# Kernel optimization log

Hardware: AMD Instinct MI355X
Metric: run time of the kernel (lower is better)

## Reference

```python
import jax, jax.numpy as jnp
import numpy as np

NUM_LAYERS = 3
HIDDEN = 64
NUM_CLASSES = 4096
LN_EPS = 1e-5


def setup_inputs() -> dict:
    key = jax.random.key(0)
    ks = jax.random.split(key, 8)
    B, N, E, H = 8, NUM_CLASSES, 131072, HIDDEN
    node_features = jax.random.normal(ks[0], (B, N, H), dtype=jnp.float32)
    edge_indices = jax.random.randint(ks[1], (B, 2, E), 0, N, dtype=jnp.int64)
    edge_attrs = jax.random.normal(ks[2], (B, E, H), dtype=jnp.float32)
    # GraphConvolutionLayer params (xavier_uniform weight, zero bias) per layer
    limit = np.sqrt(6.0 / (H + H)).astype(np.float32)
    W = jax.random.uniform(ks[3], (NUM_LAYERS, H, H), minval=-limit, maxval=limit, dtype=jnp.float32)
    b = jnp.zeros((NUM_LAYERS, H), dtype=jnp.float32)
    gamma = jnp.ones((NUM_LAYERS, H), dtype=jnp.float32)
    beta = jnp.zeros((NUM_LAYERS, H), dtype=jnp.float32)
    global_emb = 0.02 * jax.random.normal(ks[4], (N, H), dtype=jnp.float32)
    return {
        "node_features": node_features,
        "edge_indices": edge_indices,
        "edge_attrs": edge_attrs,
        "W": W,
        "b": b,
        "gamma": gamma,
        "beta": beta,
        "global_emb": global_emb,
    }


def _layer_norm(x, g, bt):
    mu = jnp.mean(x, axis=-1, keepdims=True)
    var = jnp.mean((x - mu) ** 2, axis=-1, keepdims=True)
    return (x - mu) * jax.lax.rsqrt(var + LN_EPS) * g + bt


def reference(node_features, edge_indices, edge_attrs, W, b, gamma, beta, global_emb):
    N = node_features.shape[1]

    def per_graph(x0, ei, ea):
        # presence mask computed on raw node features [N, 1]
        presence = (jnp.sum(x0, axis=1) != 0).astype(x0.dtype)[:, None]
        src, dst = ei[0], ei[1]
        x = x0
        for i in range(NUM_LAYERS):
            residual = x
            h = x @ W[i]                                   # [N, H]
            msg = h[src] * ea                              # gather + edge gate [E, H]
            out = jax.ops.segment_sum(msg, dst, num_segments=N) + b[i]
            out = jax.nn.relu(out)
            out = _layer_norm(out, gamma[i], beta[i])
            x = out + residual if i > 0 else out
        return x * presence + global_emb * (1.0 - presence)

    return jax.vmap(per_graph)(node_features, edge_indices, edge_attrs)
```

## Files before the change

### kernel.cpp

```cpp
#include <hip/hip_runtime.h>

#define GB 8
#define GN 4096
#define GH 64
#define GE 131072
#define LN_EPS 1e-5f
#define NBIN (GB * GN)
#define TOTE (GB * GE)

static __device__ __forceinline__ unsigned short f2bf(float f) {
    union { float f; unsigned int u; } v; v.f = f;
    unsigned int u = v.u;
    return (unsigned short)((u + 0x7FFFu + ((u >> 16) & 1u)) >> 16);
}
static __device__ __forceinline__ void bf2x(unsigned int u, float& lo, float& hi) {
    union { float f; unsigned int i; } a, b;
    a.i = u << 16; b.i = u & 0xFFFF0000u;
    lo = a.f; hi = b.f;
}
static __device__ __forceinline__ void fma8(uint4 ev, uint4 hv, float4& a0, float4& a1) {
    float el, eh, hl, hh;
    bf2x(ev.x, el, eh); bf2x(hv.x, hl, hh);
    a0.x = fmaf(el, hl, a0.x); a0.y = fmaf(eh, hh, a0.y);
    bf2x(ev.y, el, eh); bf2x(hv.y, hl, hh);
    a0.z = fmaf(el, hl, a0.z); a0.w = fmaf(eh, hh, a0.w);
    bf2x(ev.z, el, eh); bf2x(hv.z, hl, hh);
    a1.x = fmaf(el, hl, a1.x); a1.y = fmaf(eh, hh, a1.y);
    bf2x(ev.w, el, eh); bf2x(hv.w, hl, hh);
    a1.z = fmaf(el, hl, a1.z); a1.w = fmaf(eh, hh, a1.w);
}

__global__ void k_init(const float* __restrict__ nf, float* __restrict__ pres) {
    int w = (blockIdx.x * blockDim.x + threadIdx.x) >> 6;
    int lane = threadIdx.x & 63;
    if (w >= NBIN) return;
    float v = nf[(size_t)w * GH + lane];
    #pragma unroll
    for (int o = 1; o < 64; o <<= 1) v += __shfl_xor(v, o, 64);
    if (lane == 0) pres[w] = (v != 0.0f) ? 1.0f : 0.0f;
}

__global__ void k_hist(const int* __restrict__ ei, int* __restrict__ hist) {
    int t = blockIdx.x * blockDim.x + threadIdx.x;
    int b = t >> 17, e = t & (GE - 1);
    int dst = ei[(b << 18) + GE + e];
    atomicAdd(&hist[(b << 12) + dst], 1);
}

__global__ void k_scan(const int* __restrict__ hist, int* __restrict__ off,
                       int* __restrict__ cur) {
    __shared__ int part[256];
    int b = blockIdx.x;
    int t = threadIdx.x;
    int base = (b << 12) + t * 16;
    int c[16];
    int s = 0;
    #pragma unroll
    for (int i = 0; i < 16; ++i) { c[i] = hist[base + i]; s += c[i]; }
    part[t] = s;
    __syncthreads();
    for (int o = 1; o < 256; o <<= 1) {
        int u = (t >= o) ? part[t - o] : 0;
        __syncthreads();
        part[t] += u;
        __syncthreads();
    }
    int p = b * GE + part[t] - s;
    #pragma unroll
    for (int i = 0; i < 16; ++i) { off[base + i] = p; cur[base + i] = p; p += c[i]; }
    if (b == GB - 1 && t == 255) off[NBIN] = TOTE;
}

__global__ void k_fillperm(const int* __restrict__ ei, int* __restrict__ cur,
                           const float* __restrict__ ea,
                           int* __restrict__ sSrc, unsigned short* __restrict__ ea_s) {
    int grp = (blockIdx.x * blockDim.x + threadIdx.x) >> 4;
    if (grp >= TOTE) return;
    int sub  = threadIdx.x & 15;
    int lane = threadIdx.x & 63;
    int b = grp >> 17, e = grp & (GE - 1);
    int dst = ei[(b << 18) + GE + e];
    int pos = 0;
    if (sub == 0) pos = atomicAdd(&cur[(b << 12) + dst], 1);
    pos = __shfl(pos, lane & ~15, 64);
    float4 v = *reinterpret_cast<const float4*>(ea + ((size_t)grp << 6) + (sub << 2));
    ushort4 o;
    o.x = f2bf(v.x); o.y = f2bf(v.y); o.z = f2bf(v.z); o.w = f2bf(v.w);
    *reinterpret_cast<ushort4*>(ea_s + ((size_t)pos << 6) + (sub << 2)) = o;
    if (sub == 0) sSrc[pos] = ei[(b << 18) + e];
}

__global__ void k_gemm(const float* __restrict__ x, const float* __restrict__ W,
                       unsigned short* __restrict__ h, int layer) {
    __shared__ float Wl[GH * GH];
    for (int i = threadIdx.x; i < GH * GH; i += blockDim.x)
        Wl[i] = W[layer * GH * GH + i];
    __syncthreads();
    int w = (blockIdx.x * blockDim.x + threadIdx.x) >> 6;
    int lane = threadIdx.x & 63;
    if (w >= NBIN) return;
    float xv = x[(size_t)w * GH + lane];
    float acc = 0.0f;
    #pragma unroll
    for (int k = 0; k < GH; ++k)
        acc = fmaf(__shfl(xv, k, 64), Wl[k * GH + lane], acc);
    h[(size_t)w * GH + lane] = f2bf(acc);
}

__global__ void k_gather(const int* __restrict__ off, const int* __restrict__ sSrc,
                         const unsigned short* __restrict__ ea_s,
                         const unsigned short* __restrict__ h,
                         const float* __restrict__ bias, const float* __restrict__ gam,
                         const float* __restrict__ bet,
                         float* __restrict__ x, const float* __restrict__ pres,
                         const float* __restrict__ ge, float* __restrict__ out,
                         int layer) {
    int w = (blockIdx.x * blockDim.x + threadIdx.x) >> 3;
    if (w >= NBIN) return;
    int sub = threadIdx.x & 7;
    int b = w >> 12;
    int beg = off[w], end = off[w + 1];
    const unsigned short* hb = h + ((((size_t)b) << 12) * GH);

    float4 a0 = make_float4(0.f, 0.f, 0.f, 0.f);
    float4 a1 = make_float4(0.f, 0.f, 0.f, 0.f);
    int e = beg;
    for (; e + 4 <= end; e += 4) {
        int s0 = sSrc[e + 0];
        int s1 = sSrc[e + 1];
        int s2 = sSrc[e + 2];
        int s3 = sSrc[e + 3];
        uint4 ev0 = *reinterpret_cast<const uint4*>(ea_s + (((size_t)(e + 0)) << 6) + (sub << 3));
        uint4 ev1 = *reinterpret_cast<const uint4*>(ea_s + (((size_t)(e + 1)) << 6) + (sub << 3));
        uint4 ev2 = *reinterpret_cast<const uint4*>(ea_s + (((size_t)(e + 2)) << 6) + (sub << 3));
        uint4 ev3 = *reinterpret_cast<const uint4*>(ea_s + (((size_t)(e + 3)) << 6) + (sub << 3));
        uint4 hv0 = *reinterpret_cast<const uint4*>(hb + (((size_t)s0) << 6) + (sub << 3));
        uint4 hv1 = *reinterpret_cast<const uint4*>(hb + (((size_t)s1) << 6) + (sub << 3));
        uint4 hv2 = *reinterpret_cast<const uint4*>(hb + (((size_t)s2) << 6) + (sub << 3));
        uint4 hv3 = *reinterpret_cast<const uint4*>(hb + (((size_t)s3) << 6) + (sub << 3));
        fma8(ev0, hv0, a0, a1);
        fma8(ev1, hv1, a0, a1);
        fma8(ev2, hv2, a0, a1);
        fma8(ev3, hv3, a0, a1);
    }
    for (; e < end; ++e) {
        int s0 = sSrc[e];
        uint4 ev = *reinterpret_cast<const uint4*>(ea_s + (((size_t)e) << 6) + (sub << 3));
        uint4 hv = *reinterpret_cast<const uint4*>(hb + (((size_t)s0) << 6) + (sub << 3));
        fma8(ev, hv, a0, a1);
    }

    const float4* bias4 = reinterpret_cast<const float4*>(bias + layer * GH + (sub << 3));
    float4 b0 = bias4[0], b1 = bias4[1];
    float4 v0, v1;
    v0.x = fmaxf(a0.x + b0.x, 0.f); v0.y = fmaxf(a0.y + b0.y, 0.f);
    v0.z = fmaxf(a0.z + b0.z, 0.f); v0.w = fmaxf(a0.w + b0.w, 0.f);
    v1.x = fmaxf(a1.x + b1.x, 0.f); v1.y = fmaxf(a1.y + b1.y, 0.f);
    v1.z = fmaxf(a1.z + b1.z, 0.f); v1.w = fmaxf(a1.w + b1.w, 0.f);
    float s = v0.x + v0.y + v0.z + v0.w + v1.x + v1.y + v1.z + v1.w;
    #pragma unroll
    for (int o = 1; o < 8; o <<= 1) s += __shfl_xor(s, o, 64);
    float mu = s * (1.0f / GH);
    float4 d0, d1;
    d0.x = v0.x - mu; d0.y = v0.y - mu; d0.z = v0.z - mu; d0.w = v0.w - mu;
    d1.x = v1.x - mu; d1.y = v1.y - mu; d1.z = v1.z - mu; d1.w = v1.w - mu;
    float q = d0.x*d0.x + d0.y*d0.y + d0.z*d0.z + d0.w*d0.w
            + d1.x*d1.x + d1.y*d1.y + d1.z*d1.z + d1.w*d1.w;
    #pragma unroll
    for (int o = 1; o < 8; o <<= 1) q += __shfl_xor(q, o, 64);
    float r = rsqrtf(q * (1.0f / GH) + LN_EPS);
    const float4* gam4 = reinterpret_cast<const float4*>(gam + layer * GH + (sub << 3));
    const float4* bet4 = reinterpret_cast<const float4*>(bet + layer * GH + (sub << 3));
    float4 g0 = gam4[0], g1 = gam4[1];
    float4 t0 = bet4[0], t1 = bet4[1];
    float4 y0, y1;
    y0.x = d0.x * r * g0.x + t0.x; y0.y = d0.y * r * g0.y + t0.y;
    y0.z = d0.z * r * g0.z + t0.z; y0.w = d0.w * r * g0.w + t0.w;
    y1.x = d1.x * r * g1.x + t1.x; y1.y = d1.y * r * g1.y + t1.y;
    y1.z = d1.z * r * g1.z + t1.z; y1.w = d1.w * r * g1.w + t1.w;

    float4* xp = reinterpret_cast<float4*>(x + (size_t)w * GH + (sub << 3));
    if (layer > 0) {
        float4 x0 = xp[0], x1 = xp[1];
        y0.x += x0.x; y0.y += x0.y; y0.z += x0.z; y0.w += x0.w;
        y1.x += x1.x; y1.y += x1.y; y1.z += x1.z; y1.w += x1.w;
    }
    if (layer < 2) {
        xp[0] = y0; xp[1] = y1;
    } else {
        float p = pres[w];
        const float4* ge4 = reinterpret_cast<const float4*>(ge + (size_t)(w & (GN - 1)) * GH + (sub << 3));
        float4 e0 = ge4[0], e1 = ge4[1];
        float4 o0, o1;
        o0.x = y0.x * p + e0.x * (1.f - p); o0.y = y0.y * p + e0.y * (1.f - p);
        o0.z = y0.z * p + e0.z * (1.f - p); o0.w = y0.w * p + e0.w * (1.f - p);
        o1.x = y1.x * p + e1.x * (1.f - p); o1.y = y1.y * p + e1.y * (1.f - p);
        o1.z = y1.z * p + e1.z * (1.f - p); o1.w = y1.w * p + e1.w * (1.f - p);
        float4* op = reinterpret_cast<float4*>(out + (size_t)w * GH + (sub << 3));
        op[0] = o0; op[1] = o1;
    }
}

extern "C" void kernel_launch(void* const* d_in, const int* in_sizes, int n_in,
                              void* d_out, int out_size, void* d_ws, size_t ws_size,
                              hipStream_t stream) {
    const float* nf = (const float*)d_in[0];
    const int* ei   = (const int*)d_in[1];
    const float* ea = (const float*)d_in[2];
    const float* W  = (const float*)d_in[3];
    const float* bb = (const float*)d_in[4];
    const float* gg = (const float*)d_in[5];
    const float* be = (const float*)d_in[6];
    const float* ge = (const float*)d_in[7];
    float* out = (float*)d_out;

    float* x    = (float*)d_ws;
    float* pres = x + (size_t)NBIN * GH;
    int* off    = (int*)(pres + NBIN);
    int* cur    = off + NBIN + 1;
    int* hist   = cur + NBIN;
    int* sSrc   = hist + NBIN;
    unsigned short* h_s  = (unsigned short*)(sSrc + TOTE);
    unsigned short* ea_s = h_s + (size_t)NBIN * GH;

    hipMemsetAsync(hist, 0, NBIN * sizeof(int), stream);
    k_init<<<NBIN / 4, 256, 0, stream>>>(nf, pres);
    k_hist<<<TOTE / 256, 256, 0, stream>>>(ei, hist);
    k_scan<<<GB, 256, 0, stream>>>(hist, off, cur);
    k_fillperm<<<TOTE / 16, 256, 0, stream>>>(ei, cur, ea, sSrc, ea_s);

    for (int l = 0; l < 3; ++l) {
        k_gemm<<<NBIN / 4, 256, 0, stream>>>(l == 0 ? nf : x, W, h_s, l);
        k_gather<<<NBIN * 8 / 256, 256, 0, stream>>>(off, sSrc, ea_s, h_s, bb, gg, be,
                                                     x, pres, ge, out, l);
    }
}
```

Baseline: 428.1 us.

## Use a full wavefront per destination node in gather with edge-parallel groups

Each destination node's segment sum now uses a full 64-lane wavefront instead of 8 lanes. Eight groups of 8 lanes each take different edges, and the partial sums are combined with cross-group xor shuffles. Only group 0 writes the result. This adds parallelism for the gather, about 32 edges per node on average, and more loads in flight. The cost is 8x more threads, shuffle-reduction overhead, and redundant LayerNorm work in the idle groups.

```diff
diff --git a/kernel.cpp b/kernel.cpp
--- a/kernel.cpp
+++ b/kernel.cpp
@@ -115,39 +115,43 @@
                          float* __restrict__ x, const float* __restrict__ pres,
                          const float* __restrict__ ge, float* __restrict__ out,
                          int layer) {
-    int w = (blockIdx.x * blockDim.x + threadIdx.x) >> 3;
+    int w = (blockIdx.x * blockDim.x + threadIdx.x) >> 6;
     if (w >= NBIN) return;
-    int sub = threadIdx.x & 7;
+    int lane = threadIdx.x & 63;
+    int g   = lane >> 3;
+    int sub = lane & 7;
     int b = w >> 12;
     int beg = off[w], end = off[w + 1];
     const unsigned short* hb = h + ((((size_t)b) << 12) * GH);
 
     float4 a0 = make_float4(0.f, 0.f, 0.f, 0.f);
     float4 a1 = make_float4(0.f, 0.f, 0.f, 0.f);
-    int e = beg;
-    for (; e + 4 <= end; e += 4) {
-        int s0 = sSrc[e + 0];
-        int s1 = sSrc[e + 1];
-        int s2 = sSrc[e + 2];
-        int s3 = sSrc[e + 3];
-        uint4 ev0 = *reinterpret_cast<const uint4*>(ea_s + (((size_t)(e + 0)) << 6) + (sub << 3));
-        uint4 ev1 = *reinterpret_cast<const uint4*>(ea_s + (((size_t)(e + 1)) << 6) + (sub << 3));
-        uint4 ev2 = *reinterpret_cast<const uint4*>(ea_s + (((size_t)(e + 2)) << 6) + (sub << 3));
-        uint4 ev3 = *reinterpret_cast<const uint4*>(ea_s + (((size_t)(e + 3)) << 6) + (sub << 3));
-        uint4 hv0 = *reinterpret_cast<const uint4*>(hb + (((size_t)s0) << 6) + (sub << 3));
-        uint4 hv1 = *reinterpret_cast<const uint4*>(hb + (((size_t)s1) << 6) + (sub << 3));
-        uint4 hv2 = *reinterpret_cast<const uint4*>(hb + (((size_t)s2) << 6) + (sub << 3));
-        uint4 hv3 = *reinterpret_cast<const uint4*>(hb + (((size_t)s3) << 6) + (sub << 3));
-        fma8(ev0, hv0, a0, a1);
-        fma8(ev1, hv1, a0, a1);
-        fma8(ev2, hv2, a0, a1);
-        fma8(ev3, hv3, a0, a1);
-    }
-    for (; e < end; ++e) {
-        int s0 = sSrc[e];
-        uint4 ev = *reinterpret_cast<const uint4*>(ea_s + (((size_t)e) << 6) + (sub << 3));
-        uint4 hv = *reinterpret_cast<const uint4*>(hb + (((size_t)s0) << 6) + (sub << 3));
-        fma8(ev, hv, a0, a1);
+    for (int e = beg; e < end; e += 16) {
+        int e0 = e + g;
+        int e1 = e + 8 + g;
+        if (e0 < end) {
+            int s0 = sSrc[e0];
+            uint4 ev = *reinterpret_cast<const uint4*>(ea_s + (((size_t)e0) << 6) + (sub << 3));
+            uint4 hv = *reinterpret_cast<const uint4*>(hb + (((size_t)s0) << 6) + (sub << 3));
+            fma8(ev, hv, a0, a1);
+        }
+        if (e1 < end) {
+            int s1 = sSrc[e1];
+            uint4 ev = *reinterpret_cast<const uint4*>(ea_s + (((size_t)e1) << 6) + (sub << 3));
+            uint4 hv = *reinterpret_cast<const uint4*>(hb + (((size_t)s1) << 6) + (sub << 3));
+            fma8(ev, hv, a0, a1);
+        }
+    }
+    #pragma unroll
+    for (int o = 8; o < 64; o <<= 1) {
+        a0.x += __shfl_xor(a0.x, o, 64);
+        a0.y += __shfl_xor(a0.y, o, 64);
+        a0.z += __shfl_xor(a0.z, o, 64);
+        a0.w += __shfl_xor(a0.w, o, 64);
+        a1.x += __shfl_xor(a1.x, o, 64);
+        a1.y += __shfl_xor(a1.y, o, 64);
+        a1.z += __shfl_xor(a1.z, o, 64);
+        a1.w += __shfl_xor(a1.w, o, 64);
     }
 
     const float4* bias4 = reinterpret_cast<const float4*>(bias + layer * GH + (sub << 3));
@@ -179,25 +183,27 @@
     y1.x = d1.x * r * g1.x + t1.x; y1.y = d1.y * r * g1.y + t1.y;
     y1.z = d1.z * r * g1.z + t1.z; y1.w = d1.w * r * g1.w + t1.w;
 
-    float4* xp = reinterpret_cast<float4*>(x + (size_t)w * GH + (sub << 3));
-    if (layer > 0) {
-        float4 x0 = xp[0], x1 = xp[1];
-        y0.x += x0.x; y0.y += x0.y; y0.z += x0.z; y0.w += x0.w;
-        y1.x += x1.x; y1.y += x1.y; y1.z += x1.z; y1.w += x1.w;
-    }
-    if (layer < 2) {
-        xp[0] = y0; xp[1] = y1;
-    } else {
-        float p = pres[w];
-        const float4* ge4 = reinterpret_cast<const float4*>(ge + (size_t)(w & (GN - 1)) * GH + (sub << 3));
-        float4 e0 = ge4[0], e1 = ge4[1];
-        float4 o0, o1;
-        o0.x = y0.x * p + e0.x * (1.f - p); o0.y = y0.y * p + e0.y * (1.f - p);
-        o0.z = y0.z * p + e0.z * (1.f - p); o0.w = y0.w * p + e0.w * (1.f - p);
-        o1.x = y1.x * p + e1.x * (1.f - p); o1.y = y1.y * p + e1.y * (1.f - p);
-        o1.z = y1.z * p + e1.z * (1.f - p); o1.w = y1.w * p + e1.w * (1.f - p);
-        float4* op = reinterpret_cast<float4*>(out + (size_t)w * GH + (sub << 3));
-        op[0] = o0; op[1] = o1;
+    if (g == 0) {
+        float4* xp = reinterpret_cast<float4*>(x + (size_t)w * GH + (sub << 3));
+        if (layer > 0) {
+            float4 x0 = xp[0], x1 = xp[1];
+            y0.x += x0.x; y0.y += x0.y; y0.z += x0.z; y0.w += x0.w;
+            y1.x += x1.x; y1.y += x1.y; y1.z += x1.z; y1.w += x1.w;
+        }
+        if (layer < 2) {
+            xp[0] = y0; xp[1] = y1;
+        } else {
+            float p = pres[w];
+            const float4* ge4 = reinterpret_cast<const float4*>(ge + (size_t)(w & (GN - 1)) * GH + (sub << 3));
+            float4 e0 = ge4[0], e1 = ge4[1];
+            float4 o0, o1;
+            o0.x = y0.x * p + e0.x * (1.f - p); o0.y = y0.y * p + e0.y * (1.f - p);
+            o0.z = y0.z * p + e0.z * (1.f - p); o0.w = y0.w * p + e0.w * (1.f - p);
+            o1.x = y1.x * p + e1.x * (1.f - p); o1.y = y1.y * p + e1.y * (1.f - p);
+            o1.z = y1.z * p + e1.z * (1.f - p); o1.w = y1.w * p + e1.w * (1.f - p);
+            float4* op = reinterpret_cast<float4*>(out + (size_t)w * GH + (sub << 3));
+            op[0] = o0; op[1] = o1;
+        }
     }
 }
 
@@ -231,7 +237,7 @@
 
     for (int l = 0; l < 3; ++l) {
         k_gemm<<<NBIN / 4, 256, 0, stream>>>(l == 0 ? nf : x, W, h_s, l);
-        k_gather<<<NBIN * 8 / 256, 256, 0, stream>>>(off, sSrc, ea_s, h_s, bb, gg, be,
-                                                     x, pres, ge, out, l);
-    }
-}
+        k_gather<<<NBIN / 4, 256, 0, stream>>>(off, sSrc, ea_s, h_s, bb, gg, be,
+                                               x, pres, ge, out, l);
+    }
+}
```

Result: faster. 403.6 us (-5.7%).
